# Kernel tuning notes

Hardware: AMD Instinct MI355X
Metric: run time of the kernel (lower is better)

## Reference

```python
import jax, jax.numpy as jnp
import numpy as np

N = 50000
E = 800000
D_IN = 128
D_OUT = 128
BN_EPS = 1e-5


def setup_inputs() -> dict:
    key = jax.random.key(0)
    ks = jax.random.split(key, 9)
    feature = jax.random.normal(ks[0], (N, D_IN), dtype=jnp.float32)
    snorm_n = jax.random.uniform(ks[1], (N, 1), dtype=jnp.float32)
    edge_src = jax.random.randint(ks[2], (E,), 0, N, dtype=jnp.int32)
    edge_dst = jax.random.randint(ks[3], (E,), 0, N, dtype=jnp.int32)
    # Linear(in,out,bias=False) weights, applied as x @ W (W stored [in,out])
    s = 1.0 / np.sqrt(D_IN)
    W1 = jax.random.uniform(ks[4], (D_IN, D_OUT), jnp.float32, -s, s)
    W2 = jax.random.uniform(ks[5], (D_IN, D_OUT), jnp.float32, -s, s)
    W3 = jax.random.uniform(ks[6], (D_IN, D_OUT), jnp.float32, -s, s)
    bias = jnp.zeros((D_OUT,), jnp.float32)
    gamma = jnp.ones((D_OUT,), jnp.float32)
    beta = jnp.zeros((D_OUT,), jnp.float32)
    return {"feature": feature, "snorm_n": snorm_n, "W1": W1, "W2": W2,
            "W3": W3, "bias": bias, "gamma": gamma, "beta": beta,
            "edge_src": edge_src, "edge_dst": edge_dst}


def _mpconv(feat, norm, edge_src, edge_dst):
    # feat: [N, D]; norm: [N, 1] = clamp(in_deg,1)^-0.5
    h = feat * norm
    msg = h[edge_src]                                   # gather [E, D]
    agg = jax.ops.segment_sum(msg, edge_dst, num_segments=N)  # scatter-add
    return agg * norm


def reference(feature, snorm_n, W1, W2, W3, bias, gamma, beta,
              edge_src, edge_dst):
    # in-degree normalization (same graph for both MP passes)
    deg = jax.ops.segment_sum(jnp.ones_like(edge_dst, jnp.float32),
                              edge_dst, num_segments=N)
    norm = jnp.power(jnp.clip(deg, 1.0, None), -0.5)[:, None]  # [N,1]

    h_in = feature
    ax = _mpconv(feature, norm, edge_src, edge_dst)
    ax2 = _mpconv(ax, norm, edge_src, edge_dst)

    h = (feature @ W1) + ((-ax) @ W2) + ((2.0 * ax2 - feature) @ W3) + bias
    h = h * snorm_n  # graph_norm

    # BatchNorm1d over nodes (training-mode batch statistics, biased var)
    mean = jnp.mean(h, axis=0)
    var = jnp.mean(jnp.square(h - mean), axis=0)
    h = (h - mean) * jax.lax.rsqrt(var + BN_EPS) * gamma + beta

    h = jax.nn.relu(h)      # activation
    h = h_in + h            # residual (in_dim == out_dim)
    # dropout p=0.0 -> identity
    return h
```

## Files before the change

kernel.cpp:

```cpp
#include <hip/hip_runtime.h>
#include <hip/hip_bf16.h>

#define NN 50000
#define NE 800000
#define DD 128
#define BN_EPS 1e-5f
#define SCAN_G 98

typedef unsigned short ushort_t;
typedef unsigned int uint_t;
typedef __attribute__((ext_vector_type(8))) short short8v;
typedef __attribute__((ext_vector_type(4))) float f32x4;

__device__ __forceinline__ float b2f(ushort_t u) {
    union { uint_t i; float f; } v; v.i = ((uint_t)u) << 16; return v.f;
}
__device__ __forceinline__ ushort_t f2b(float f) {
    uint_t u = __float_as_uint(f);
    u += 0x7FFFu + ((u >> 16) & 1u);
    return (ushort_t)(u >> 16);
}
__device__ __forceinline__ void atomAdd(float* p, float v) { unsafeAtomicAdd(p, v); }

__global__ void epos_kernel(const int* __restrict__ dst, int* __restrict__ cnt,
                            int* __restrict__ epos) {
    int e = blockIdx.x * 256 + threadIdx.x;
    if (e < NE) epos[e] = atomicAdd(&cnt[dst[e]], 1);
}

__global__ __launch_bounds__(512) void scan_part(const int* __restrict__ deg,
                                                 int* __restrict__ part,
                                                 float* __restrict__ norm) {
    int i = blockIdx.x * 512 + threadIdx.x;
    int v = (i < NN) ? deg[i] : 0;
    if (i < NN) norm[i] = rsqrtf((float)max(v, 1));
    int s = v;
    #pragma unroll
    for (int k = 1; k < 64; k <<= 1) s += __shfl_xor(s, k);
    __shared__ int wsum[8];
    if ((threadIdx.x & 63) == 0) wsum[threadIdx.x >> 6] = s;
    __syncthreads();
    if (threadIdx.x == 0) {
        int t = 0;
        #pragma unroll
        for (int k = 0; k < 8; ++k) t += wsum[k];
        part[blockIdx.x] = t;
    }
}

__global__ __launch_bounds__(128) void scan_mid(const int* __restrict__ part,
                                                int* __restrict__ base) {
    __shared__ int sh[128];
    int t = threadIdx.x;
    sh[t] = (t < SCAN_G) ? part[t] : 0;
    __syncthreads();
    for (int s = 1; s < 128; s <<= 1) {
        int u = (t >= s) ? sh[t - s] : 0;
        __syncthreads();
        sh[t] += u;
        __syncthreads();
    }
    base[t] = t ? sh[t - 1] : 0;
}

__global__ __launch_bounds__(512) void scan_final(const int* __restrict__ deg,
                                                  const int* __restrict__ base,
                                                  int* __restrict__ off) {
    int i = blockIdx.x * 512 + threadIdx.x;
    int lane = threadIdx.x & 63, wv = threadIdx.x >> 6;
    int v = (i < NN) ? deg[i] : 0;
    int incl = v;
    #pragma unroll
    for (int s = 1; s < 64; s <<= 1) {
        int u = __shfl_up(incl, s);
        if (lane >= s) incl += u;
    }
    __shared__ int wsum[8];
    if (lane == 63) wsum[wv] = incl;
    __syncthreads();
    int woff = 0;
    for (int k = 0; k < wv; ++k) woff += wsum[k];
    int excl = base[blockIdx.x] + woff + incl - v;
    if (i < NN) off[i] = excl;
    if (blockIdx.x == 0 && threadIdx.x == 0) off[NN] = NE;
}

__global__ void fill_kernel(const int* __restrict__ src, const int* __restrict__ dst,
                            const int* __restrict__ epos, const int* __restrict__ off,
                            const float* __restrict__ norm, int2* __restrict__ csr) {
    int e = blockIdx.x * 256 + threadIdx.x;
    if (e >= NE) return;
    int s = src[e];
    int p = off[dst[e]] + epos[e];
    csr[p] = make_int2(s, __float_as_int(norm[s]));
}

__global__ void f2bf_kernel(const float* __restrict__ in, ushort_t* __restrict__ out) {
    int i = blockIdx.x * 256 + threadIdx.x;
    if (i >= NN * DD / 4) return;
    float4 v = reinterpret_cast<const float4*>(in)[i];
    ushort4 o = { f2b(v.x), f2b(v.y), f2b(v.z), f2b(v.w) };
    reinterpret_cast<ushort4*>(out)[i] = o;
}

__global__ void wct_kernel(const float* __restrict__ W1, const float* __restrict__ W2,
                           const float* __restrict__ W3, ushort_t* __restrict__ wcT) {
    int i = blockIdx.x * 256 + threadIdx.x;
    if (i >= DD * 384) return;
    int d = i / 384, k = i % 384;
    float v;
    if (k < 128)      v = W1[k * DD + d] - W3[k * DD + d];
    else if (k < 256) v = -W2[(k - 128) * DD + d];
    else              v = 2.0f * W3[(k - 256) * DD + d];
    wcT[i] = f2b(v);
}

__global__ __launch_bounds__(256) void gather_bf(const ushort_t* __restrict__ x,
                                                 const float* __restrict__ norm,
                                                 const int* __restrict__ off,
                                                 const int2* __restrict__ csr,
                                                 ushort_t* __restrict__ out) {
    int wid = (blockIdx.x << 2) + (threadIdx.x >> 6);
    int lane = threadIdx.x & 63;
    int h = lane >> 5, l5 = lane & 31;
    int jb = off[wid], je = off[wid + 1];
    const uint2* xp = reinterpret_cast<const uint2*>(x);
    float a0 = 0.f, a1 = 0.f, a2 = 0.f, a3 = 0.f;
    int j = jb;
    for (; j + 8 <= je; j += 8) {
        int e = j + (h << 2);
        int2 c0 = csr[e + 0];
        int2 c1 = csr[e + 1];
        int2 c2 = csr[e + 2];
        int2 c3 = csr[e + 3];
        uint2 v0 = xp[c0.x * 32 + l5];
        uint2 v1 = xp[c1.x * 32 + l5];
        uint2 v2 = xp[c2.x * 32 + l5];
        uint2 v3 = xp[c3.x * 32 + l5];
        float n0 = __int_as_float(c0.y), n1 = __int_as_float(c1.y);
        float n2 = __int_as_float(c2.y), n3 = __int_as_float(c3.y);
        a0 = fmaf(n0, b2f((ushort_t)v0.x), a0);
        a1 = fmaf(n0, b2f((ushort_t)(v0.x >> 16)), a1);
        a2 = fmaf(n0, b2f((ushort_t)v0.y), a2);
        a3 = fmaf(n0, b2f((ushort_t)(v0.y >> 16)), a3);
        a0 = fmaf(n1, b2f((ushort_t)v1.x), a0);
        a1 = fmaf(n1, b2f((ushort_t)(v1.x >> 16)), a1);
        a2 = fmaf(n1, b2f((ushort_t)v1.y), a2);
        a3 = fmaf(n1, b2f((ushort_t)(v1.y >> 16)), a3);
        a0 = fmaf(n2, b2f((ushort_t)v2.x), a0);
        a1 = fmaf(n2, b2f((ushort_t)(v2.x >> 16)), a1);
        a2 = fmaf(n2, b2f((ushort_t)v2.y), a2);
        a3 = fmaf(n2, b2f((ushort_t)(v2.y >> 16)), a3);
        a0 = fmaf(n3, b2f((ushort_t)v3.x), a0);
        a1 = fmaf(n3, b2f((ushort_t)(v3.x >> 16)), a1);
        a2 = fmaf(n3, b2f((ushort_t)v3.y), a2);
        a3 = fmaf(n3, b2f((ushort_t)(v3.y >> 16)), a3);
    }
    for (; j + 2 <= je; j += 2) {
        int2 c = csr[j + h];
        uint2 v = xp[c.x * 32 + l5];
        float n = __int_as_float(c.y);
        a0 = fmaf(n, b2f((ushort_t)v.x), a0);
        a1 = fmaf(n, b2f((ushort_t)(v.x >> 16)), a1);
        a2 = fmaf(n, b2f((ushort_t)v.y), a2);
        a3 = fmaf(n, b2f((ushort_t)(v.y >> 16)), a3);
    }
    if (j < je && h == 0) {
        int2 c = csr[j];
        uint2 v = xp[c.x * 32 + l5];
        float n = __int_as_float(c.y);
        a0 = fmaf(n, b2f((ushort_t)v.x), a0);
        a1 = fmaf(n, b2f((ushort_t)(v.x >> 16)), a1);
        a2 = fmaf(n, b2f((ushort_t)v.y), a2);
        a3 = fmaf(n, b2f((ushort_t)(v.y >> 16)), a3);
    }
    a0 += __shfl_xor(a0, 32);
    a1 += __shfl_xor(a1, 32);
    a2 += __shfl_xor(a2, 32);
    a3 += __shfl_xor(a3, 32);
    if (h == 0) {
        float nd = norm[wid];
        uint2 o;
        o.x = (uint_t)f2b(nd * a0) | ((uint_t)f2b(nd * a1) << 16);
        o.y = (uint_t)f2b(nd * a2) | ((uint_t)f2b(nd * a3) << 16);
        reinterpret_cast<uint2*>(out)[wid * 32 + l5] = o;
    }
}

__global__ __launch_bounds__(256) void gemm_bn(
    const ushort_t* __restrict__ feat_bf, const ushort_t* __restrict__ ax_bf,
    const ushort_t* __restrict__ ax2_bf, const ushort_t* __restrict__ wcT,
    const float* __restrict__ bias, const float* __restrict__ snorm,
    ushort_t* __restrict__ t_out, float* __restrict__ gsums, float* __restrict__ gsq)
{
    __shared__ ushort_t As[64 * 128];
    __shared__ ushort_t Bs[128 * 128];
    int tid = threadIdx.x;
    int w = tid >> 6, lane = tid & 63;
    int row0 = blockIdx.x * 64;

    f32x4 acc[8] = {};

    #pragma unroll
    for (int kt = 0; kt < 3; ++kt) {
        const ushort_t* S = (kt == 0) ? feat_bf : (kt == 1) ? ax_bf : ax2_bf;
        __syncthreads();
        {
            int r = tid >> 2, q = tid & 3;
            int grow = min(row0 + r, NN - 1);
            const char* gsrc = (const char*)(S + grow * DD);
            char* dbase = (char*)As + r * 256;
            int sw = (r & 7) << 4;
            #pragma unroll
            for (int c = 0; c < 4; ++c) {
                int cb = (q * 4 + c) * 16;
                *(short8v*)(dbase + (cb ^ sw)) = *(const short8v*)(gsrc + cb);
            }
        }
        {
            int cidx = tid >> 1, hh = tid & 1;
            const char* gsrc = (const char*)(wcT + cidx * 384 + kt * 128);
            char* dbase = (char*)Bs + cidx * 256;
            int sw = (cidx & 7) << 4;
            #pragma unroll
            for (int c = 0; c < 8; ++c) {
                int cb = (hh * 8 + c) * 16;
                *(short8v*)(dbase + (cb ^ sw)) = *(const short8v*)(gsrc + cb);
            }
        }
        __syncthreads();
        int arow = w * 16 + (lane & 15);
        int asw = (arow & 7) << 4;
        #pragma unroll
        for (int ks = 0; ks < 4; ++ks) {
            int kb = ks * 64 + ((lane >> 4) << 4);
            short8v a = *(const short8v*)((const char*)As + arow * 256 + (kb ^ asw));
            #pragma unroll
            for (int cf = 0; cf < 8; ++cf) {
                int col = cf * 16 + (lane & 15);
                short8v b = *(const short8v*)((const char*)Bs + col * 256 + (kb ^ ((col & 7) << 4)));
                acc[cf] = __builtin_amdgcn_mfma_f32_16x16x32_bf16(a, b, acc[cf], 0, 0, 0);
            }
        }
    }

    int q = lane >> 4, c0 = lane & 15;
    int rbase = row0 + w * 16 + q * 4;
    float sn[4];
    #pragma unroll
    for (int i = 0; i < 4; ++i) sn[i] = (rbase + i < NN) ? snorm[rbase + i] : 0.f;

    float s1[8], s2[8];
    #pragma unroll
    for (int cf = 0; cf < 8; ++cf) {
        s1[cf] = 0.f; s2[cf] = 0.f;
        int col = cf * 16 + c0;
        float bc = bias[col];
        #pragma unroll
        for (int i = 0; i < 4; ++i) {
            int row = rbase + i;
            if (row < NN) {
                float t = (acc[cf][i] + bc) * sn[i];
                t_out[row * DD + col] = f2b(t);
                s1[cf] += t; s2[cf] += t * t;
            }
        }
    }
    #pragma unroll
    for (int cf = 0; cf < 8; ++cf) {
        s1[cf] += __shfl_xor(s1[cf], 16); s1[cf] += __shfl_xor(s1[cf], 32);
        s2[cf] += __shfl_xor(s2[cf], 16); s2[cf] += __shfl_xor(s2[cf], 32);
    }
    if (q == 0) {
        int slot = (blockIdx.x & 31) * DD;
        #pragma unroll
        for (int cf = 0; cf < 8; ++cf) {
            atomAdd(&gsums[slot + cf * 16 + c0], s1[cf]);
            atomAdd(&gsq[slot + cf * 16 + c0], s2[cf]);
        }
    }
}

__global__ void bn_finalize(const float* __restrict__ gsums, const float* __restrict__ gsq,
                            const float* __restrict__ gamma,
                            const float* __restrict__ beta,
                            float* __restrict__ scale, float* __restrict__ shift) {
    int d = threadIdx.x;
    float s1 = 0.f, s2 = 0.f;
    for (int c = 0; c < 32; ++c) { s1 += gsums[c * DD + d]; s2 += gsq[c * DD + d]; }
    float mean = s1 / (float)NN;
    float var  = s2 / (float)NN - mean * mean;
    float sc = gamma[d] * rsqrtf(var + BN_EPS);
    scale[d] = sc;
    shift[d] = beta[d] - mean * sc;
}

__global__ void epilogue(const ushort_t* __restrict__ t, const ushort_t* __restrict__ featb,
                         const float* __restrict__ scale, const float* __restrict__ shift,
                         float* __restrict__ out) {
    int i = blockIdx.x * 256 + threadIdx.x;
    if (i >= NN * DD / 4) return;
    int d0 = (i << 2) & 127;
    ushort4 tv = reinterpret_cast<const ushort4*>(t)[i];
    ushort4 fv = reinterpret_cast<const ushort4*>(featb)[i];
    float4 o;
    o.x = b2f(fv.x) + fmaxf(b2f(tv.x) * scale[d0 + 0] + shift[d0 + 0], 0.f);
    o.y = b2f(fv.y) + fmaxf(b2f(tv.y) * scale[d0 + 1] + shift[d0 + 1], 0.f);
    o.z = b2f(fv.z) + fmaxf(b2f(tv.z) * scale[d0 + 2] + shift[d0 + 2], 0.f);
    o.w = b2f(fv.w) + fmaxf(b2f(tv.w) * scale[d0 + 3] + shift[d0 + 3], 0.f);
    reinterpret_cast<float4*>(out)[i] = o;
}

extern "C" void kernel_launch(void* const* d_in, const int* in_sizes, int n_in,
                              void* d_out, int out_size, void* d_ws, size_t ws_size,
                              hipStream_t stream) {
    const float* feat  = (const float*)d_in[0];
    const float* snorm = (const float*)d_in[1];
    const float* W1    = (const float*)d_in[2];
    const float* W2    = (const float*)d_in[3];
    const float* W3    = (const float*)d_in[4];
    const float* bias  = (const float*)d_in[5];
    const float* gamma = (const float*)d_in[6];
    const float* beta  = (const float*)d_in[7];
    const int* esrc = (const int*)d_in[8];
    const int* edst = (const int*)d_in[9];
    float* out = (float*)d_out;

    char* ws = (char*)d_ws;
    ushort_t* t_bf    = (ushort_t*)(ws);
    int*      epos    = (int*)     (ws);
    ushort_t* feat_bf = (ushort_t*)(ws + 12800000);
    ushort_t* ax_bf   = (ushort_t*)(ws + 25600000);
    ushort_t* ax2_bf  = (ushort_t*)(ws + 38400000);
    int2*     csr     = (int2*)    (ws + 51200000);
    float*    norm    = (float*)   (ws + 57600000);
    int*      cnt     = (int*)     (ws + 57800000);
    float*    gsums   = (float*)   (ws + 58000000);
    float*    gsq     = (float*)   (ws + 58016384);
    int*      off     = (int*)     (ws + 58032768);
    int*      part    = (int*)     (ws + 58232832);
    int*      base    = (int*)     (ws + 58233344);
    float*    scale   = (float*)   (ws + 58233856);
    float*    shift   = (float*)   (ws + 58234368);
    ushort_t* wcT     = (ushort_t*)(ws + 58234880);

    hipMemsetAsync(ws + 57800000, 0, 232768, stream);

    epos_kernel<<<3125, 256, 0, stream>>>(edst, cnt, epos);
    scan_part  <<<SCAN_G, 512, 0, stream>>>(cnt, part, norm);
    scan_mid   <<<1, 128, 0, stream>>>(part, base);
    scan_final <<<SCAN_G, 512, 0, stream>>>(cnt, base, off);
    fill_kernel<<<3125, 256, 0, stream>>>(esrc, edst, epos, off, norm, csr);

    f2bf_kernel<<<6250, 256, 0, stream>>>(feat, feat_bf);
    wct_kernel <<<192,  256, 0, stream>>>(W1, W2, W3, wcT);

    gather_bf<<<12500, 256, 0, stream>>>(feat_bf, norm, off, csr, ax_bf);
    gather_bf<<<12500, 256, 0, stream>>>(ax_bf,   norm, off, csr, ax2_bf);

    gemm_bn<<<782, 256, 0, stream>>>(feat_bf, ax_bf, ax2_bf, wcT, bias, snorm,
                                     t_bf, gsums, gsq);
    bn_finalize<<<1, 128, 0, stream>>>(gsums, gsq, gamma, beta, scale, shift);
    epilogue   <<<6250, 256, 0, stream>>>(t_bf, feat_bf, scale, shift, out);
}
```

Measured before the change: 185.4 us.

## Fuse scan and prep kernels, nontemporal CSR loads, 128-row GEMM tiles

Folds the middle scan step into scan_final, so each block sums the preceding partials itself, and merges the bf16 feature conversion and weight-transpose kernels into one launch. This removes two kernel launches. CSR edge loads in the gather now use nontemporal hints to reduce cache pollution. The GEMM tile grows from 64 to 128 rows per block with two accumulator sets, halving the grid, reusing B fragments and cutting BN atomics, at the cost of more LDS and registers per block.

```diff
diff --git a/kernel.cpp b/kernel.cpp
--- a/kernel.cpp
+++ b/kernel.cpp
@@ -21,6 +21,11 @@
     return (ushort_t)(u >> 16);
 }
 __device__ __forceinline__ void atomAdd(float* p, float v) { unsafeAtomicAdd(p, v); }
+__device__ __forceinline__ int2 ldnt2(const int2* p) {
+    unsigned long long v =
+        __builtin_nontemporal_load(reinterpret_cast<const unsigned long long*>(p));
+    int2 r; r.x = (int)(v & 0xFFFFFFFFull); r.y = (int)(v >> 32); return r;
+}
 
 __global__ void epos_kernel(const int* __restrict__ dst, int* __restrict__ cnt,
                             int* __restrict__ epos) {
@@ -48,26 +53,28 @@
     }
 }
 
-__global__ __launch_bounds__(128) void scan_mid(const int* __restrict__ part,
-                                                int* __restrict__ base) {
-    __shared__ int sh[128];
+__global__ __launch_bounds__(512) void scan_final(const int* __restrict__ deg,
+                                                  const int* __restrict__ part,
+                                                  int* __restrict__ off) {
+    __shared__ int wsum[8];
+    __shared__ int sbase;
     int t = threadIdx.x;
-    sh[t] = (t < SCAN_G) ? part[t] : 0;
-    __syncthreads();
-    for (int s = 1; s < 128; s <<= 1) {
-        int u = (t >= s) ? sh[t - s] : 0;
-        __syncthreads();
-        sh[t] += u;
-        __syncthreads();
-    }
-    base[t] = t ? sh[t - 1] : 0;
-}
-
-__global__ __launch_bounds__(512) void scan_final(const int* __restrict__ deg,
-                                                  const int* __restrict__ base,
-                                                  int* __restrict__ off) {
-    int i = blockIdx.x * 512 + threadIdx.x;
-    int lane = threadIdx.x & 63, wv = threadIdx.x >> 6;
+    int lane = t & 63, wv = t >> 6;
+
+    int p = (t < blockIdx.x && t < SCAN_G) ? part[t] : 0;
+    #pragma unroll
+    for (int s = 1; s < 64; s <<= 1) p += __shfl_xor(p, s);
+    if (lane == 0) wsum[wv] = p;
+    __syncthreads();
+    if (t == 0) {
+        int b = 0;
+        #pragma unroll
+        for (int k = 0; k < 8; ++k) b += wsum[k];
+        sbase = b;
+    }
+    __syncthreads();
+
+    int i = blockIdx.x * 512 + t;
     int v = (i < NN) ? deg[i] : 0;
     int incl = v;
     #pragma unroll
@@ -75,14 +82,14 @@
         int u = __shfl_up(incl, s);
         if (lane >= s) incl += u;
     }
-    __shared__ int wsum[8];
+    __syncthreads();
     if (lane == 63) wsum[wv] = incl;
     __syncthreads();
     int woff = 0;
     for (int k = 0; k < wv; ++k) woff += wsum[k];
-    int excl = base[blockIdx.x] + woff + incl - v;
+    int excl = sbase + woff + incl - v;
     if (i < NN) off[i] = excl;
-    if (blockIdx.x == 0 && threadIdx.x == 0) off[NN] = NE;
+    if (blockIdx.x == 0 && t == 0) off[NN] = NE;
 }
 
 __global__ void fill_kernel(const int* __restrict__ src, const int* __restrict__ dst,
@@ -95,24 +102,25 @@
     csr[p] = make_int2(s, __float_as_int(norm[s]));
 }
 
-__global__ void f2bf_kernel(const float* __restrict__ in, ushort_t* __restrict__ out) {
-    int i = blockIdx.x * 256 + threadIdx.x;
-    if (i >= NN * DD / 4) return;
-    float4 v = reinterpret_cast<const float4*>(in)[i];
-    ushort4 o = { f2b(v.x), f2b(v.y), f2b(v.z), f2b(v.w) };
-    reinterpret_cast<ushort4*>(out)[i] = o;
-}
-
-__global__ void wct_kernel(const float* __restrict__ W1, const float* __restrict__ W2,
-                           const float* __restrict__ W3, ushort_t* __restrict__ wcT) {
-    int i = blockIdx.x * 256 + threadIdx.x;
-    if (i >= DD * 384) return;
-    int d = i / 384, k = i % 384;
-    float v;
-    if (k < 128)      v = W1[k * DD + d] - W3[k * DD + d];
-    else if (k < 256) v = -W2[(k - 128) * DD + d];
-    else              v = 2.0f * W3[(k - 256) * DD + d];
-    wcT[i] = f2b(v);
+__global__ void prep_kernel(const float* __restrict__ feat, ushort_t* __restrict__ feat_bf,
+                            const float* __restrict__ W1, const float* __restrict__ W2,
+                            const float* __restrict__ W3, ushort_t* __restrict__ wcT) {
+    int b = blockIdx.x;
+    if (b < 6250) {
+        int i = b * 256 + threadIdx.x;
+        float4 v = reinterpret_cast<const float4*>(feat)[i];
+        ushort4 o = { f2b(v.x), f2b(v.y), f2b(v.z), f2b(v.w) };
+        reinterpret_cast<ushort4*>(feat_bf)[i] = o;
+    } else {
+        int i = (b - 6250) * 256 + threadIdx.x;
+        if (i >= DD * 384) return;
+        int d = i / 384, k = i % 384;
+        float v;
+        if (k < 128)      v = W1[k * DD + d] - W3[k * DD + d];
+        else if (k < 256) v = -W2[(k - 128) * DD + d];
+        else              v = 2.0f * W3[(k - 256) * DD + d];
+        wcT[i] = f2b(v);
+    }
 }
 
 __global__ __launch_bounds__(256) void gather_bf(const ushort_t* __restrict__ x,
@@ -129,10 +137,10 @@
     int j = jb;
     for (; j + 8 <= je; j += 8) {
         int e = j + (h << 2);
-        int2 c0 = csr[e + 0];
-        int2 c1 = csr[e + 1];
-        int2 c2 = csr[e + 2];
-        int2 c3 = csr[e + 3];
+        int2 c0 = ldnt2(&csr[e + 0]);
+        int2 c1 = ldnt2(&csr[e + 1]);
+        int2 c2 = ldnt2(&csr[e + 2]);
+        int2 c3 = ldnt2(&csr[e + 3]);
         uint2 v0 = xp[c0.x * 32 + l5];
         uint2 v1 = xp[c1.x * 32 + l5];
         uint2 v2 = xp[c2.x * 32 + l5];
@@ -157,7 +165,7 @@
         a3 = fmaf(n3, b2f((ushort_t)(v3.y >> 16)), a3);
     }
     for (; j + 2 <= je; j += 2) {
-        int2 c = csr[j + h];
+        int2 c = ldnt2(&csr[j + h]);
         uint2 v = xp[c.x * 32 + l5];
         float n = __int_as_float(c.y);
         a0 = fmaf(n, b2f((ushort_t)v.x), a0);
@@ -166,7 +174,7 @@
         a3 = fmaf(n, b2f((ushort_t)(v.y >> 16)), a3);
     }
     if (j < je && h == 0) {
-        int2 c = csr[j];
+        int2 c = ldnt2(&csr[j]);
         uint2 v = xp[c.x * 32 + l5];
         float n = __int_as_float(c.y);
         a0 = fmaf(n, b2f((ushort_t)v.x), a0);
@@ -193,27 +201,27 @@
     const float* __restrict__ bias, const float* __restrict__ snorm,
     ushort_t* __restrict__ t_out, float* __restrict__ gsums, float* __restrict__ gsq)
 {
-    __shared__ ushort_t As[64 * 128];
+    __shared__ ushort_t As[128 * 128];
     __shared__ ushort_t Bs[128 * 128];
     int tid = threadIdx.x;
     int w = tid >> 6, lane = tid & 63;
-    int row0 = blockIdx.x * 64;
-
-    f32x4 acc[8] = {};
+    int row0 = blockIdx.x * 128;
+
+    f32x4 acc[2][8] = {};
 
     #pragma unroll
     for (int kt = 0; kt < 3; ++kt) {
         const ushort_t* S = (kt == 0) ? feat_bf : (kt == 1) ? ax_bf : ax2_bf;
         __syncthreads();
         {
-            int r = tid >> 2, q = tid & 3;
+            int r = tid >> 1, hh = tid & 1;
             int grow = min(row0 + r, NN - 1);
             const char* gsrc = (const char*)(S + grow * DD);
             char* dbase = (char*)As + r * 256;
             int sw = (r & 7) << 4;
             #pragma unroll
-            for (int c = 0; c < 4; ++c) {
-                int cb = (q * 4 + c) * 16;
+            for (int c = 0; c < 8; ++c) {
+                int cb = hh * 128 + c * 16;
                 *(short8v*)(dbase + (cb ^ sw)) = *(const short8v*)(gsrc + cb);
             }
         }
@@ -224,45 +232,52 @@
             int sw = (cidx & 7) << 4;
             #pragma unroll
             for (int c = 0; c < 8; ++c) {
-                int cb = (hh * 8 + c) * 16;
+                int cb = hh * 128 + c * 16;
                 *(short8v*)(dbase + (cb ^ sw)) = *(const short8v*)(gsrc + cb);
             }
         }
         __syncthreads();
-        int arow = w * 16 + (lane & 15);
-        int asw = (arow & 7) << 4;
+        int l15 = lane & 15;
+        int r0a = w * 32 + l15;
+        int r1a = r0a + 16;
         #pragma unroll
         for (int ks = 0; ks < 4; ++ks) {
             int kb = ks * 64 + ((lane >> 4) << 4);
-            short8v a = *(const short8v*)((const char*)As + arow * 256 + (kb ^ asw));
+            short8v a0 = *(const short8v*)((const char*)As + r0a * 256 + (kb ^ ((r0a & 7) << 4)));
+            short8v a1 = *(const short8v*)((const char*)As + r1a * 256 + (kb ^ ((r1a & 7) << 4)));
             #pragma unroll
             for (int cf = 0; cf < 8; ++cf) {
-                int col = cf * 16 + (lane & 15);
+                int col = cf * 16 + l15;
                 short8v b = *(const short8v*)((const char*)Bs + col * 256 + (kb ^ ((col & 7) << 4)));
-                acc[cf] = __builtin_amdgcn_mfma_f32_16x16x32_bf16(a, b, acc[cf], 0, 0, 0);
+                acc[0][cf] = __builtin_amdgcn_mfma_f32_16x16x32_bf16(a0, b, acc[0][cf], 0, 0, 0);
+                acc[1][cf] = __builtin_amdgcn_mfma_f32_16x16x32_bf16(a1, b, acc[1][cf], 0, 0, 0);
             }
         }
     }
 
     int q = lane >> 4, c0 = lane & 15;
-    int rbase = row0 + w * 16 + q * 4;
-    float sn[4];
-    #pragma unroll
-    for (int i = 0; i < 4; ++i) sn[i] = (rbase + i < NN) ? snorm[rbase + i] : 0.f;
-
     float s1[8], s2[8];
     #pragma unroll
-    for (int cf = 0; cf < 8; ++cf) {
-        s1[cf] = 0.f; s2[cf] = 0.f;
-        int col = cf * 16 + c0;
-        float bc = bias[col];
-        #pragma unroll
-        for (int i = 0; i < 4; ++i) {
-            int row = rbase + i;
-            if (row < NN) {
-                float t = (acc[cf][i] + bc) * sn[i];
-                t_out[row * DD + col] = f2b(t);
-                s1[cf] += t; s2[cf] += t * t;
+    for (int cf = 0; cf < 8; ++cf) { s1[cf] = 0.f; s2[cf] = 0.f; }
+
+    #pragma unroll
+    for (int g = 0; g < 2; ++g) {
+        int rbase = row0 + w * 32 + g * 16 + q * 4;
+        float sn[4];
+        #pragma unroll
+        for (int i = 0; i < 4; ++i) sn[i] = (rbase + i < NN) ? snorm[rbase + i] : 0.f;
+        #pragma unroll
+        for (int cf = 0; cf < 8; ++cf) {
+            int col = cf * 16 + c0;
+            float bc = bias[col];
+            #pragma unroll
+            for (int i = 0; i < 4; ++i) {
+                int row = rbase + i;
+                if (row < NN) {
+                    float t = (acc[g][cf][i] + bc) * sn[i];
+                    t_out[row * DD + col] = f2b(t);
+                    s1[cf] += t; s2[cf] += t * t;
+                }
             }
         }
     }
@@ -339,7 +354,6 @@
     float*    gsq     = (float*)   (ws + 58016384);
     int*      off     = (int*)     (ws + 58032768);
     int*      part    = (int*)     (ws + 58232832);
-    int*      base    = (int*)     (ws + 58233344);
     float*    scale   = (float*)   (ws + 58233856);
     float*    shift   = (float*)   (ws + 58234368);
     ushort_t* wcT     = (ushort_t*)(ws + 58234880);
@@ -348,17 +362,15 @@
 
     epos_kernel<<<3125, 256, 0, stream>>>(edst, cnt, epos);
     scan_part  <<<SCAN_G, 512, 0, stream>>>(cnt, part, norm);
-    scan_mid   <<<1, 128, 0, stream>>>(part, base);
-    scan_final <<<SCAN_G, 512, 0, stream>>>(cnt, base, off);
+    scan_final <<<SCAN_G, 512, 0, stream>>>(cnt, part, off);
     fill_kernel<<<3125, 256, 0, stream>>>(esrc, edst, epos, off, norm, csr);
 
-    f2bf_kernel<<<6250, 256, 0, stream>>>(feat, feat_bf);
-    wct_kernel <<<192,  256, 0, stream>>>(W1, W2, W3, wcT);
+    prep_kernel<<<6442, 256, 0, stream>>>(feat, feat_bf, W1, W2, W3, wcT);
 
     gather_bf<<<12500, 256, 0, stream>>>(feat_bf, norm, off, csr, ax_bf);
     gather_bf<<<12500, 256, 0, stream>>>(ax_bf,   norm, off, csr, ax2_bf);
 
-    gemm_bn<<<782, 256, 0, stream>>>(feat_bf, ax_bf, ax2_bf, wcT, bias, snorm,
+    gemm_bn<<<391, 256, 0, stream>>>(feat_bf, ax_bf, ax2_bf, wcT, bias, snorm,
                                      t_bf, gsums, gsq);
     bn_finalize<<<1, 128, 0, stream>>>(gsums, gsq, gamma, beta, scale, shift);
     epilogue   <<<6250, 256, 0, stream>>>(t_bf, feat_bf, scale, shift, out);
```

Result: slower. 193.0 us (+4.1%).
